# Optimization experiments

Hardware: AMD Instinct MI355X
Metric: run time of the kernel (lower is better)

Reference implementation:

```python
import jax, jax.numpy as jnp
import numpy as np

N = 50000   # num nodes
E = 800000  # num edges (avg degree 16)
D = 128     # in = hidden = out channels


def setup_inputs() -> dict:
    key = jax.random.key(0)
    k0, k1, k2, k3, k4, k5 = jax.random.split(key, 6)
    x = jax.random.normal(k0, (N, D), dtype=jnp.float32)
    edge_index = jax.random.randint(k1, (2, E), 0, N, dtype=jnp.int32)
    scale = 1.0 / np.sqrt(D)
    W1 = jax.random.normal(k2, (D, D), dtype=jnp.float32) * scale
    b1 = jax.random.normal(k3, (D,), dtype=jnp.float32) * 0.01
    W2 = jax.random.normal(k4, (D, D), dtype=jnp.float32) * scale
    b2 = jax.random.normal(k5, (D,), dtype=jnp.float32) * 0.01
    return {"x": x, "edge_index": edge_index, "W1": W1, "b1": b1, "W2": W2, "b2": b2}


def reference(x, edge_index, W1, b1, W2, b2):
    n = x.shape[0]
    src, dst = edge_index[0], edge_index[1]
    # GCN adds self-loops before normalization
    loops = jnp.arange(n, dtype=src.dtype)
    s = jnp.concatenate([src, loops])
    d = jnp.concatenate([dst, loops])
    # symmetric normalization: deg^{-1/2}[s] * deg^{-1/2}[d]
    deg = jax.ops.segment_sum(jnp.ones_like(d, dtype=x.dtype), d, num_segments=n)
    dinv = jnp.where(deg > 0, jax.lax.rsqrt(deg), 0.0)
    ew = dinv[s] * dinv[d]  # [E+N]

    def gcn_conv(h, W, b):
        h = h @ W                                   # [N, D] dense transform first
        msg = ew[:, None] * h[s]                     # gather over edges [E+N, D]
        agg = jax.ops.segment_sum(msg, d, num_segments=n)  # scatter-add [N, D]
        return agg + b

    # layer 1: conv -> Identity BN -> ELU (dropout=0.0 -> no-op)
    h = jax.nn.elu(gcn_conv(x, W1, b1))
    # layer 2 (last): conv -> Identity BN -> ELU
    out = jax.nn.elu(gcn_conv(h, W2, b2))
    return out
```

## Files before the change

kernel.cpp:

```cpp
#include <hip/hip_runtime.h>
#include <math.h>

#define D 128
#define BCAP 8192
#define SLICE 64
#define PB 256

typedef __attribute__((ext_vector_type(8))) short bf16x8;
typedef __attribute__((ext_vector_type(4))) float f32x4;
typedef __attribute__((ext_vector_type(4))) unsigned int u32x4;


__device__ inline float2 bf2f2(unsigned int u) {
    union { unsigned int i; float f; } a, b;
    a.i = u << 16;
    b.i = u & 0xffff0000u;
    return make_float2(a.f, b.f);
}

__device__ inline unsigned short f2bf(float f) {
    union { float f; unsigned int i; } u;
    u.f = f;
    unsigned int r = u.i + 0x7fffu + ((u.i >> 16) & 1u);
    return (unsigned short)(r >> 16);
}


__device__ __forceinline__ void gemm_core(unsigned short (*Ws)[136], int gbid,
                                          const void* __restrict__ Ain, int a_fp32,
                                          unsigned int* __restrict__ Cb, int N) {
    const int tid = threadIdx.x;
    const int wid = tid >> 6;
    const int lane = tid & 63;
    const int quad = lane >> 4;
    const int ln = lane & 15;
    const int m = gbid * 64 + wid * 16 + ln;
    const bool valid = (m < N);

    f32x4 acc[8];
#pragma unroll
    for (int c = 0; c < 8; ++c) acc[c] = (f32x4){0.f, 0.f, 0.f, 0.f};

    __syncthreads();

#pragma unroll
    for (int ks = 0; ks < 4; ++ks) {
        const int k0 = ks * 32;
        bf16x8 af;
        if (a_fp32) {
            const float* A = (const float*)Ain;
            float4 lo = make_float4(0.f, 0.f, 0.f, 0.f), hi = lo;
            if (valid) {
                lo = *(const float4*)&A[(size_t)m * 128 + k0 + quad * 8];
                hi = *(const float4*)&A[(size_t)m * 128 + k0 + quad * 8 + 4];
            }
            af[0] = (short)f2bf(lo.x); af[1] = (short)f2bf(lo.y);
            af[2] = (short)f2bf(lo.z); af[3] = (short)f2bf(lo.w);
            af[4] = (short)f2bf(hi.x); af[5] = (short)f2bf(hi.y);
            af[6] = (short)f2bf(hi.z); af[7] = (short)f2bf(hi.w);
        } else {
            const uint4* A4 = (const uint4*)Ain;
            uint4 v = valid ? A4[(size_t)m * 16 + ks * 4 + quad]
                            : make_uint4(0u, 0u, 0u, 0u);
            union { uint4 u; bf16x8 h; } cv;
            cv.u = v;
            af = cv.h;
        }
#pragma unroll
        for (int c = 0; c < 8; ++c) {
            bf16x8 bf = *(const bf16x8*)&Ws[c * 16 + ln][k0 + quad * 8];
            acc[c] = __builtin_amdgcn_mfma_f32_16x16x32_bf16(af, bf, acc[c], 0, 0, 0);
        }
    }

    const int rowbase = gbid * 64 + wid * 16 + quad * 4;
#pragma unroll
    for (int c = 0; c < 8; ++c) {
#pragma unroll
        for (int r = 0; r < 4; ++r) {
            float v = acc[c][r];
            float vn = __shfl_xor(v, 1);
            int grow = rowbase + r;
            if (!(ln & 1) && grow < N) {
                unsigned int u = (unsigned int)f2bf(v) | ((unsigned int)f2bf(vn) << 16);
                Cb[(size_t)grow * 64 + c * 8 + (ln >> 1)] = u;
            }
        }
    }
}


__global__ __launch_bounds__(256) void k1_all(
        const int* __restrict__ src, const int* __restrict__ dst,
        const float* __restrict__ x, const float* __restrict__ W1,
        const float* __restrict__ W2, unsigned short* __restrict__ Wt2,
        unsigned int* __restrict__ pairs, unsigned char* __restrict__ cellCnt,
        unsigned int* __restrict__ hb1, int e, int chunk, int N, int gemmBlocks) {
    __shared__ __align__(16) unsigned char smem[128 * 136 * 2];
    const int tid = threadIdx.x;
    const int bid = blockIdx.x;

    if (bid < PB) {
        int* cur = (int*)smem;
        cur[tid] = 0;
        __syncthreads();
        const int e0 = bid * chunk;
        const int e1 = min(e0 + chunk, e);
        for (int i = e0 + tid; i < e1; i += 256) {
            int d = dst[i], s = src[i];
            int b = d >> 8;
            int off = atomicAdd(&cur[b], 1);
            if (off < SLICE)
                pairs[((size_t)(bid * 256 + b)) * SLICE + off] =
                    (unsigned int)s | ((unsigned int)(d & 255) << 16);
        }
        __syncthreads();
        cellCnt[bid * 256 + tid] = (unsigned char)min(cur[tid], SLICE);
    } else if (bid < PB + gemmBlocks) {
        unsigned short (*Ws)[136] = (unsigned short(*)[136])smem;
        for (int j = 0; j < 64; ++j) {
            int idx = tid + j * 256;
            Ws[idx & 127][idx >> 7] = f2bf(W1[idx]);
        }
        gemm_core(Ws, bid - PB, x, 1, hb1, N);
    } else {
        int i = (bid - PB - gemmBlocks) * 256 + tid;
        int k = i >> 7, n = i & 127;
        Wt2[n * 128 + k] = f2bf(W2[i]);
    }
}


__global__ __launch_bounds__(256) void partB(const unsigned int* __restrict__ pairs,
                                             const unsigned char* __restrict__ cellCnt,
                                             unsigned short* __restrict__ col,
                                             unsigned int* __restrict__ meta,
                                             float* __restrict__ dinv, int n) {
    __shared__ int deg[256];
    __shared__ int sc[256];
    __shared__ int cur[256];
    const int b = blockIdx.x;
    const int tid = threadIdx.x;

    deg[tid] = 0;
    __syncthreads();

    const int c = cellCnt[tid * 256 + b];
    const unsigned int* cell = pairs + ((size_t)(tid * 256 + b)) * SLICE;
    for (int q = 0; q < c; ++q) atomicAdd(&deg[cell[q] >> 16], 1);
    __syncthreads();

    int v = deg[tid];
    sc[tid] = v;
    __syncthreads();
    for (int o = 1; o < 256; o <<= 1) {
        int t = (tid >= o) ? sc[tid - o] : 0;
        __syncthreads();
        sc[tid] += t;
        __syncthreads();
    }
    int startw = sc[tid] - v;
    cur[tid] = startw;

    int node = b * 256 + tid;
    if (node < n) {
        meta[node] = ((unsigned int)(b * BCAP + startw) << 10) | (unsigned int)v;
        dinv[node] = rsqrtf((float)(v + 1));
    }
    __syncthreads();

    for (int q = 0; q < c; ++q) {
        unsigned int p = cell[q];
        int dl = p >> 16;
        int off = atomicAdd(&cur[dl], 1);
        col[(size_t)b * BCAP + off] = (unsigned short)(p & 0xffffu);
    }
}


__device__ __forceinline__ void fma8(float w, u32x4 u, f32x4& a, f32x4& b) {
    float2 v0 = bf2f2(u.x), v1 = bf2f2(u.y), v2 = bf2f2(u.z), v3 = bf2f2(u.w);
    a[0] = fmaf(w, v0.x, a[0]); a[1] = fmaf(w, v0.y, a[1]);
    a[2] = fmaf(w, v1.x, a[2]); a[3] = fmaf(w, v1.y, a[3]);
    b[0] = fmaf(w, v2.x, b[0]); b[1] = fmaf(w, v2.y, b[1]);
    b[2] = fmaf(w, v3.x, b[2]); b[3] = fmaf(w, v3.y, b[3]);
}

__device__ __forceinline__ void agg_wave(const unsigned int* __restrict__ hb,
                                         const unsigned short* __restrict__ col,
                                         const float* __restrict__ dinv,
                                         int node, int g, int ln,
                                         unsigned int m, float di,
                                         f32x4& sA, f32x4& sB) {
    const u32x4* hb4 = (const u32x4*)hb;
    const int s0 = (int)(m >> 10);
    const int s1 = s0 + (int)(m & 1023u);

    {
        u32x4 su = hb4[(size_t)node * 16 + ln];
        float ws = (g == 0) ? di : 0.f;
        fma8(ws, su, sA, sB);
    }

    int i = s0;
    for (; i + 16 <= s1; i += 16) {
        const int c0 = col[i + g];
        const int c1 = col[i + 4 + g];
        const int c2 = col[i + 8 + g];
        const int c3 = col[i + 12 + g];
        const float w0 = dinv[c0], w1 = dinv[c1], w2 = dinv[c2], w3 = dinv[c3];
        u32x4 u0 = hb4[(size_t)c0 * 16 + ln];
        u32x4 u1 = hb4[(size_t)c1 * 16 + ln];
        u32x4 u2 = hb4[(size_t)c2 * 16 + ln];
        u32x4 u3 = hb4[(size_t)c3 * 16 + ln];
        asm volatile("" :: "v"(u0), "v"(u1), "v"(u2), "v"(u3));
        fma8(w0, u0, sA, sB);
        fma8(w1, u1, sA, sB);
        fma8(w2, u2, sA, sB);
        fma8(w3, u3, sA, sB);
    }
    while (i < s1) {
        const int t = i + g;
        const int cc = (t < s1) ? (int)col[t] : node;
        const float w = (t < s1) ? dinv[cc] : 0.f;
        u32x4 u = hb4[(size_t)cc * 16 + ln];
        fma8(w, u, sA, sB);
        i += 4;
    }

#pragma unroll
    for (int k = 0; k < 4; ++k) {
        sA[k] += __shfl_xor(sA[k], 16);
        sA[k] += __shfl_xor(sA[k], 32);
        sB[k] += __shfl_xor(sB[k], 16);
        sB[k] += __shfl_xor(sB[k], 32);
    }
}


__global__ __launch_bounds__(1024, 4) void k3_agg_gemm(
        const unsigned int* __restrict__ hb1, const unsigned int* __restrict__ meta,
        const unsigned short* __restrict__ col, const float* __restrict__ dinv,
        const float* __restrict__ b1, const unsigned short* __restrict__ Wt2,
        unsigned int* __restrict__ hb2, int n) {
    __shared__ unsigned int g1s[16 * 68];
    __shared__ __align__(16) unsigned short Ws[128][136];

    const int tid = threadIdx.x;
    const int wid = tid >> 6;
    const int lane = tid & 63;
    const int g = lane >> 4;
    const int ln = lane & 15;
    const int nodeBase = blockIdx.x * 16;
    const int node = nodeBase + wid;

    {
        const int nloc = tid >> 3;
        const int kb = (tid & 7) * 16;
        const uint4* gp = (const uint4*)(Wt2 + (size_t)nloc * 128 + kb);
        uint4* sp = (uint4*)&Ws[nloc][kb];
        sp[0] = gp[0];
        sp[1] = gp[1];
    }

    f32x4 sA = (f32x4){0.f, 0.f, 0.f, 0.f};
    f32x4 sB = (f32x4){0.f, 0.f, 0.f, 0.f};
    if (node < n) {
        const unsigned int m = meta[node];
        const float di = dinv[node];
        agg_wave(hb1, col, dinv, node, g, ln, m, di, sA, sB);

        const float4 bA = ((const float4*)b1)[2 * ln];
        const float4 bB = ((const float4*)b1)[2 * ln + 1];
        float r0 = fmaf(di, sA[0], bA.x), r1 = fmaf(di, sA[1], bA.y);
        float r2 = fmaf(di, sA[2], bA.z), r3 = fmaf(di, sA[3], bA.w);
        float r4 = fmaf(di, sB[0], bB.x), r5 = fmaf(di, sB[1], bB.y);
        float r6 = fmaf(di, sB[2], bB.z), r7 = fmaf(di, sB[3], bB.w);
        r0 = r0 > 0.f ? r0 : expm1f(r0); r1 = r1 > 0.f ? r1 : expm1f(r1);
        r2 = r2 > 0.f ? r2 : expm1f(r2); r3 = r3 > 0.f ? r3 : expm1f(r3);
        r4 = r4 > 0.f ? r4 : expm1f(r4); r5 = r5 > 0.f ? r5 : expm1f(r5);
        r6 = r6 > 0.f ? r6 : expm1f(r6); r7 = r7 > 0.f ? r7 : expm1f(r7);
        if (g == 0) {
            g1s[wid * 68 + ln * 4 + 0] = (unsigned int)f2bf(r0) | ((unsigned int)f2bf(r1) << 16);
            g1s[wid * 68 + ln * 4 + 1] = (unsigned int)f2bf(r2) | ((unsigned int)f2bf(r3) << 16);
            g1s[wid * 68 + ln * 4 + 2] = (unsigned int)f2bf(r4) | ((unsigned int)f2bf(r5) << 16);
            g1s[wid * 68 + ln * 4 + 3] = (unsigned int)f2bf(r6) | ((unsigned int)f2bf(r7) << 16);
        }
    } else if (g == 0) {
        g1s[wid * 68 + ln * 4 + 0] = 0u;
        g1s[wid * 68 + ln * 4 + 1] = 0u;
        g1s[wid * 68 + ln * 4 + 2] = 0u;
        g1s[wid * 68 + ln * 4 + 3] = 0u;
    }
    __syncthreads();

    if (wid < 8) {
        const int quad = lane >> 4;
        f32x4 acc = (f32x4){0.f, 0.f, 0.f, 0.f};
#pragma unroll
        for (int ks = 0; ks < 4; ++ks) {
            bf16x8 af = *(const bf16x8*)&g1s[ln * 68 + ks * 16 + quad * 4];
            bf16x8 bf = *(const bf16x8*)&Ws[wid * 16 + ln][ks * 32 + quad * 8];
            acc = __builtin_amdgcn_mfma_f32_16x16x32_bf16(af, bf, acc, 0, 0, 0);
        }
#pragma unroll
        for (int r = 0; r < 4; ++r) {
            float v = acc[r];
            float vn = __shfl_xor(v, 1);
            int grow = nodeBase + quad * 4 + r;
            if (!(ln & 1) && grow < n) {
                hb2[(size_t)grow * 64 + wid * 8 + (ln >> 1)] =
                    (unsigned int)f2bf(v) | ((unsigned int)f2bf(vn) << 16);
            }
        }
    }
}


__global__ __launch_bounds__(256, 4) void agg_elu(const unsigned int* __restrict__ hb,
                                                  const unsigned int* __restrict__ meta,
                                                  const unsigned short* __restrict__ col,
                                                  const float* __restrict__ dinv,
                                                  const float* __restrict__ bias,
                                                  float* __restrict__ outf, int n) {
    const int wid = threadIdx.x >> 6;
    const int lane = threadIdx.x & 63;
    const int g = lane >> 4;
    const int ln = lane & 15;
    const int node = blockIdx.x * 4 + wid;
    if (node >= n) return;

    const unsigned int m = meta[node];
    const float di = dinv[node];
    f32x4 sA = (f32x4){0.f, 0.f, 0.f, 0.f};
    f32x4 sB = (f32x4){0.f, 0.f, 0.f, 0.f};
    agg_wave(hb, col, dinv, node, g, ln, m, di, sA, sB);

    if (g == 0) {
        const float4 bA = ((const float4*)bias)[2 * ln];
        const float4 bB = ((const float4*)bias)[2 * ln + 1];
        float4 rA, rB;
        rA.x = fmaf(di, sA[0], bA.x); rA.y = fmaf(di, sA[1], bA.y);
        rA.z = fmaf(di, sA[2], bA.z); rA.w = fmaf(di, sA[3], bA.w);
        rB.x = fmaf(di, sB[0], bB.x); rB.y = fmaf(di, sB[1], bB.y);
        rB.z = fmaf(di, sB[2], bB.z); rB.w = fmaf(di, sB[3], bB.w);
        rA.x = rA.x > 0.f ? rA.x : expm1f(rA.x);
        rA.y = rA.y > 0.f ? rA.y : expm1f(rA.y);
        rA.z = rA.z > 0.f ? rA.z : expm1f(rA.z);
        rA.w = rA.w > 0.f ? rA.w : expm1f(rA.w);
        rB.x = rB.x > 0.f ? rB.x : expm1f(rB.x);
        rB.y = rB.y > 0.f ? rB.y : expm1f(rB.y);
        rB.z = rB.z > 0.f ? rB.z : expm1f(rB.z);
        rB.w = rB.w > 0.f ? rB.w : expm1f(rB.w);
        ((float4*)outf)[(size_t)node * 32 + 2 * ln] = rA;
        ((float4*)outf)[(size_t)node * 32 + 2 * ln + 1] = rB;
    }
}


extern "C" void kernel_launch(void* const* d_in, const int* in_sizes, int n_in,
                              void* d_out, int out_size, void* d_ws, size_t ws_size,
                              hipStream_t stream) {
    const float* x  = (const float*)d_in[0];
    const int*   ei = (const int*)d_in[1];
    const float* W1 = (const float*)d_in[2];
    const float* b1 = (const float*)d_in[3];
    const float* W2 = (const float*)d_in[4];
    const float* b2 = (const float*)d_in[5];
    float* out = (float*)d_out;

    const int N = in_sizes[0] / D;
    const int E = in_sizes[1] / 2;
    const int* src = ei;
    const int* dst = ei + E;
    const int NB = (N + 255) / 256;

    char* ws = (char*)d_ws;
    size_t off = 0;
    auto alloc = [&](size_t bytes) -> void* {
        void* p = ws + off;
        off = (off + bytes + 255) & ~(size_t)255;
        return p;
    };
    unsigned int*   pairs   = (unsigned int*)alloc((size_t)PB * 256 * SLICE * 4);
    unsigned char*  cellCnt = (unsigned char*)alloc((size_t)PB * 256);
    unsigned short* col     = (unsigned short*)alloc((size_t)NB * BCAP * 2);
    unsigned int*   meta    = (unsigned int*)alloc((size_t)N * 4);
    float*          dinv    = (float*)alloc((size_t)N * 4);
    unsigned short* Wt2     = (unsigned short*)alloc(128 * 128 * 2);
    unsigned int*   hb1     = (unsigned int*)alloc((size_t)N * 64 * 4);
    unsigned int*   hb2     = (unsigned int*)alloc((size_t)N * 64 * 4);
    (void)ws_size; (void)n_in; (void)out_size;

    const int chunk = (E + PB - 1) / PB;
    const int gemmBlocks = (N + 63) / 64;

    k1_all<<<PB + gemmBlocks + 64, 256, 0, stream>>>(src, dst, x, W1, W2, Wt2,
                                                     pairs, cellCnt, hb1, E, chunk,
                                                     N, gemmBlocks);
    partB<<<NB, 256, 0, stream>>>(pairs, cellCnt, col, meta, dinv, N);
    k3_agg_gemm<<<(N + 15) / 16, 1024, 0, stream>>>(hb1, meta, col, dinv, b1, Wt2, hb2, N);
    agg_elu<<<(N + 3) / 4, 256, 0, stream>>>(hb2, meta, col, dinv, b2, out, N);
}
```

Measured before the change: 191.7 us.

## Pre-scale layer-2 features by dinv, use reduce-scatter shuffles and fast ELU

The layer-2 GEMM epilogue now multiplies each output row by its dinv before storing, so the second aggregation can sum neighbour rows without gathering dinv per edge. The cross-group shuffle reduction becomes a reduce-scatter, so all four lane groups each finish two columns and write them, instead of one group writing eight. ELU now uses __expf(x)-1 in place of expm1f, and index arithmetic drops to 32-bit shifts. This removes per-edge dinv loads and redundant epilogue work, at the cost of extra bf16 rounding on the pre-scaled values and lower ELU accuracy near zero.

```diff
diff --git a/kernel.cpp b/kernel.cpp
--- a/kernel.cpp
+++ b/kernel.cpp
@@ -23,6 +23,10 @@
     u.f = f;
     unsigned int r = u.i + 0x7fffu + ((u.i >> 16) & 1u);
     return (unsigned short)(r >> 16);
+}
+
+__device__ __forceinline__ float elu_fast(float r) {
+    return r > 0.f ? r : __expf(r) - 1.f;
 }
 
 
@@ -186,19 +190,27 @@
     b[2] = fmaf(w, v3.x, b[2]); b[3] = fmaf(w, v3.y, b[3]);
 }
 
-__device__ __forceinline__ void agg_wave(const unsigned int* __restrict__ hb,
-                                         const unsigned short* __restrict__ col,
-                                         const float* __restrict__ dinv,
-                                         int node, int g, int ln,
-                                         unsigned int m, float di,
-                                         f32x4& sA, f32x4& sB) {
+__device__ __forceinline__ void add8(u32x4 u, f32x4& a, f32x4& b) {
+    float2 v0 = bf2f2(u.x), v1 = bf2f2(u.y), v2 = bf2f2(u.z), v3 = bf2f2(u.w);
+    a[0] += v0.x; a[1] += v0.y; a[2] += v1.x; a[3] += v1.y;
+    b[0] += v2.x; b[1] += v2.y; b[2] += v3.x; b[3] += v3.y;
+}
+
+template <bool PRE>
+__device__ __forceinline__ float2 agg_wave_rs(const unsigned int* __restrict__ hb,
+                                              const unsigned short* __restrict__ col,
+                                              const float* __restrict__ dinv,
+                                              int node, int g, int ln,
+                                              unsigned int m, float di) {
     const u32x4* hb4 = (const u32x4*)hb;
     const int s0 = (int)(m >> 10);
     const int s1 = s0 + (int)(m & 1023u);
 
+    f32x4 sA = (f32x4){0.f, 0.f, 0.f, 0.f};
+    f32x4 sB = (f32x4){0.f, 0.f, 0.f, 0.f};
     {
-        u32x4 su = hb4[(size_t)node * 16 + ln];
-        float ws = (g == 0) ? di : 0.f;
+        u32x4 su = hb4[((unsigned)node << 4) + ln];
+        float ws = (g == 0) ? (PRE ? 1.f : di) : 0.f;
         fma8(ws, su, sA, sB);
     }
 
@@ -208,33 +220,49 @@
         const int c1 = col[i + 4 + g];
         const int c2 = col[i + 8 + g];
         const int c3 = col[i + 12 + g];
-        const float w0 = dinv[c0], w1 = dinv[c1], w2 = dinv[c2], w3 = dinv[c3];
-        u32x4 u0 = hb4[(size_t)c0 * 16 + ln];
-        u32x4 u1 = hb4[(size_t)c1 * 16 + ln];
-        u32x4 u2 = hb4[(size_t)c2 * 16 + ln];
-        u32x4 u3 = hb4[(size_t)c3 * 16 + ln];
+        float w0 = 0.f, w1 = 0.f, w2 = 0.f, w3 = 0.f;
+        if (!PRE) { w0 = dinv[c0]; w1 = dinv[c1]; w2 = dinv[c2]; w3 = dinv[c3]; }
+        u32x4 u0 = hb4[((unsigned)c0 << 4) + ln];
+        u32x4 u1 = hb4[((unsigned)c1 << 4) + ln];
+        u32x4 u2 = hb4[((unsigned)c2 << 4) + ln];
+        u32x4 u3 = hb4[((unsigned)c3 << 4) + ln];
         asm volatile("" :: "v"(u0), "v"(u1), "v"(u2), "v"(u3));
-        fma8(w0, u0, sA, sB);
-        fma8(w1, u1, sA, sB);
-        fma8(w2, u2, sA, sB);
-        fma8(w3, u3, sA, sB);
+        if (PRE) {
+            add8(u0, sA, sB); add8(u1, sA, sB);
+            add8(u2, sA, sB); add8(u3, sA, sB);
+        } else {
+            fma8(w0, u0, sA, sB); fma8(w1, u1, sA, sB);
+            fma8(w2, u2, sA, sB); fma8(w3, u3, sA, sB);
+        }
     }
     while (i < s1) {
         const int t = i + g;
-        const int cc = (t < s1) ? (int)col[t] : node;
-        const float w = (t < s1) ? dinv[cc] : 0.f;
-        u32x4 u = hb4[(size_t)cc * 16 + ln];
-        fma8(w, u, sA, sB);
+        const bool ok = (t < s1);
+        const int cc = ok ? (int)col[t] : node;
+        u32x4 u = hb4[((unsigned)cc << 4) + ln];
+        if (PRE) {
+            if (ok) add8(u, sA, sB);
+        } else {
+            const float w = ok ? dinv[cc] : 0.f;
+            fma8(w, u, sA, sB);
+        }
         i += 4;
     }
 
+    f32x4 t;
 #pragma unroll
     for (int k = 0; k < 4; ++k) {
-        sA[k] += __shfl_xor(sA[k], 16);
-        sA[k] += __shfl_xor(sA[k], 32);
-        sB[k] += __shfl_xor(sB[k], 16);
-        sB[k] += __shfl_xor(sB[k], 32);
-    }
+        float pa = __shfl_xor(sA[k], 16);
+        float pb = __shfl_xor(sB[k], 16);
+        t[k] = (g & 1) ? (sB[k] + pb) : (sA[k] + pa);
+    }
+    float p0 = __shfl_xor(t[0], 32);
+    float p1 = __shfl_xor(t[1], 32);
+    float p2 = __shfl_xor(t[2], 32);
+    float p3 = __shfl_xor(t[3], 32);
+    float e0 = (g & 2) ? (t[2] + p2) : (t[0] + p0);
+    float e1 = (g & 2) ? (t[3] + p3) : (t[1] + p1);
+    return make_float2(e0, e1);
 }
 
 
@@ -263,34 +291,17 @@
         sp[1] = gp[1];
     }
 
-    f32x4 sA = (f32x4){0.f, 0.f, 0.f, 0.f};
-    f32x4 sB = (f32x4){0.f, 0.f, 0.f, 0.f};
+    const int cp = 4 * ln + 2 * (g & 1) + (g >> 1);
     if (node < n) {
         const unsigned int m = meta[node];
         const float di = dinv[node];
-        agg_wave(hb1, col, dinv, node, g, ln, m, di, sA, sB);
-
-        const float4 bA = ((const float4*)b1)[2 * ln];
-        const float4 bB = ((const float4*)b1)[2 * ln + 1];
-        float r0 = fmaf(di, sA[0], bA.x), r1 = fmaf(di, sA[1], bA.y);
-        float r2 = fmaf(di, sA[2], bA.z), r3 = fmaf(di, sA[3], bA.w);
-        float r4 = fmaf(di, sB[0], bB.x), r5 = fmaf(di, sB[1], bB.y);
-        float r6 = fmaf(di, sB[2], bB.z), r7 = fmaf(di, sB[3], bB.w);
-        r0 = r0 > 0.f ? r0 : expm1f(r0); r1 = r1 > 0.f ? r1 : expm1f(r1);
-        r2 = r2 > 0.f ? r2 : expm1f(r2); r3 = r3 > 0.f ? r3 : expm1f(r3);
-        r4 = r4 > 0.f ? r4 : expm1f(r4); r5 = r5 > 0.f ? r5 : expm1f(r5);
-        r6 = r6 > 0.f ? r6 : expm1f(r6); r7 = r7 > 0.f ? r7 : expm1f(r7);
-        if (g == 0) {
-            g1s[wid * 68 + ln * 4 + 0] = (unsigned int)f2bf(r0) | ((unsigned int)f2bf(r1) << 16);
-            g1s[wid * 68 + ln * 4 + 1] = (unsigned int)f2bf(r2) | ((unsigned int)f2bf(r3) << 16);
-            g1s[wid * 68 + ln * 4 + 2] = (unsigned int)f2bf(r4) | ((unsigned int)f2bf(r5) << 16);
-            g1s[wid * 68 + ln * 4 + 3] = (unsigned int)f2bf(r6) | ((unsigned int)f2bf(r7) << 16);
-        }
-    } else if (g == 0) {
-        g1s[wid * 68 + ln * 4 + 0] = 0u;
-        g1s[wid * 68 + ln * 4 + 1] = 0u;
-        g1s[wid * 68 + ln * 4 + 2] = 0u;
-        g1s[wid * 68 + ln * 4 + 3] = 0u;
+        float2 e = agg_wave_rs<false>(hb1, col, dinv, node, g, ln, m, di);
+        const float2 bv = ((const float2*)b1)[cp];
+        float r0 = elu_fast(fmaf(di, e.x, bv.x));
+        float r1 = elu_fast(fmaf(di, e.y, bv.y));
+        g1s[wid * 68 + cp] = (unsigned int)f2bf(r0) | ((unsigned int)f2bf(r1) << 16);
+    } else {
+        g1s[wid * 68 + cp] = 0u;
     }
     __syncthreads();
 
@@ -305,9 +316,10 @@
         }
 #pragma unroll
         for (int r = 0; r < 4; ++r) {
-            float v = acc[r];
+            int grow = nodeBase + quad * 4 + r;
+            float dsc = (grow < n) ? dinv[grow] : 0.f;
+            float v = acc[r] * dsc;
             float vn = __shfl_xor(v, 1);
-            int grow = nodeBase + quad * 4 + r;
             if (!(ln & 1) && grow < n) {
                 hb2[(size_t)grow * 64 + wid * 8 + (ln >> 1)] =
                     (unsigned int)f2bf(v) | ((unsigned int)f2bf(vn) << 16);
@@ -332,29 +344,14 @@
 
     const unsigned int m = meta[node];
     const float di = dinv[node];
-    f32x4 sA = (f32x4){0.f, 0.f, 0.f, 0.f};
-    f32x4 sB = (f32x4){0.f, 0.f, 0.f, 0.f};
-    agg_wave(hb, col, dinv, node, g, ln, m, di, sA, sB);
-
-    if (g == 0) {
-        const float4 bA = ((const float4*)bias)[2 * ln];
-        const float4 bB = ((const float4*)bias)[2 * ln + 1];
-        float4 rA, rB;
-        rA.x = fmaf(di, sA[0], bA.x); rA.y = fmaf(di, sA[1], bA.y);
-        rA.z = fmaf(di, sA[2], bA.z); rA.w = fmaf(di, sA[3], bA.w);
-        rB.x = fmaf(di, sB[0], bB.x); rB.y = fmaf(di, sB[1], bB.y);
-        rB.z = fmaf(di, sB[2], bB.z); rB.w = fmaf(di, sB[3], bB.w);
-        rA.x = rA.x > 0.f ? rA.x : expm1f(rA.x);
-        rA.y = rA.y > 0.f ? rA.y : expm1f(rA.y);
-        rA.z = rA.z > 0.f ? rA.z : expm1f(rA.z);
-        rA.w = rA.w > 0.f ? rA.w : expm1f(rA.w);
-        rB.x = rB.x > 0.f ? rB.x : expm1f(rB.x);
-        rB.y = rB.y > 0.f ? rB.y : expm1f(rB.y);
-        rB.z = rB.z > 0.f ? rB.z : expm1f(rB.z);
-        rB.w = rB.w > 0.f ? rB.w : expm1f(rB.w);
-        ((float4*)outf)[(size_t)node * 32 + 2 * ln] = rA;
-        ((float4*)outf)[(size_t)node * 32 + 2 * ln + 1] = rB;
-    }
+    float2 e = agg_wave_rs<true>(hb, col, dinv, node, g, ln, m, di);
+
+    const int cp = 4 * ln + 2 * (g & 1) + (g >> 1);
+    const float2 bv = ((const float2*)bias)[cp];
+    float2 r;
+    r.x = elu_fast(fmaf(di, e.x, bv.x));
+    r.y = elu_fast(fmaf(di, e.y, bv.y));
+    ((float2*)outf)[(size_t)node * 64 + cp] = r;
 }
 
 
```

New measurement: 189.2 us. About the same (-1.3%).
